# Kernel optimization log

Measured on AMD Instinct MI355X. Metric: run time of the kernel, lower is better.

The kernel has to match this reference:

```python
import jax, jax.numpy as jnp
import numpy as np

H = 128  # GRU hidden size


def gru_cell(x_t, h, W_ih, W_hh, b_ih, b_hh):
    # Standard torch GRU cell math.
    gi = x_t @ W_ih.T + b_ih            # (bs, 3H)
    gh = h @ W_hh.T + b_hh              # (bs, 3H)
    i_r, i_z, i_n = jnp.split(gi, 3, axis=-1)
    h_r, h_z, h_n = jnp.split(gh, 3, axis=-1)
    r = jax.nn.sigmoid(i_r + h_r)
    z = jax.nn.sigmoid(i_z + h_z)
    n = jnp.tanh(i_n + r * h_n)
    return (1.0 - z) * n + z * h


def setup_inputs() -> dict:
    key = jax.random.key(0)
    ks = jax.random.split(key, 16)
    bs, seq, emb, nc = 64, 1024, 300, 23
    s = 0.05
    inp = {
        "x": jax.random.normal(ks[0], (bs, seq, emb), jnp.float32),
        "adj": jax.random.uniform(ks[1], (bs, seq, seq), jnp.float32),
        "mask": jax.random.uniform(ks[2], (bs, seq, 1), jnp.float32),
        # GRU forward direction params (torch layout: W_ih (3H, emb), W_hh (3H, H))
        "W_ih_f": jax.random.normal(ks[3], (3 * H, emb), jnp.float32) * s,
        "W_hh_f": jax.random.normal(ks[4], (3 * H, H), jnp.float32) * s,
        "b_ih_f": jax.random.normal(ks[5], (3 * H,), jnp.float32) * s,
        "b_hh_f": jax.random.normal(ks[6], (3 * H,), jnp.float32) * s,
        # GRU backward direction params
        "W_ih_b": jax.random.normal(ks[7], (3 * H, emb), jnp.float32) * s,
        "W_hh_b": jax.random.normal(ks[8], (3 * H, H), jnp.float32) * s,
        "b_ih_b": jax.random.normal(ks[9], (3 * H,), jnp.float32) * s,
        "b_hh_b": jax.random.normal(ks[10], (3 * H,), jnp.float32) * s,
        # MLP head: Linear(300+256,128) -> Linear(128,64) -> Linear(64,23)
        "W1": jax.random.normal(ks[11], (128, emb + 2 * H), jnp.float32) * s,
        "b1": jnp.zeros((128,), jnp.float32),
        "W2": jax.random.normal(ks[12], (64, 128), jnp.float32) * s,
        "b2": jnp.zeros((64,), jnp.float32),
        "W3": jax.random.normal(ks[13], (nc, 64), jnp.float32) * s,
        "b3": jnp.zeros((nc,), jnp.float32),
    }
    return inp


def reference(x, adj, mask, W_ih_f, W_hh_f, b_ih_f, b_hh_f,
              W_ih_b, W_hh_b, b_ih_b, b_hh_b, W1, b1, W2, b2, W3, b3):
    x = x * mask                                   # (bs, seq, emb)
    bs, seq, emb = x.shape

    # --- bidirectional GRU, last-step output ---
    # Forward direction output at t = seq-1 is the final hidden of a full scan.
    h0 = jnp.zeros((bs, H), x.dtype)
    def step(h, x_t):
        h_new = gru_cell(x_t, h, W_ih_f, W_hh_f, b_ih_f, b_hh_f)
        return h_new, None
    h_fwd, _ = jax.lax.scan(step, h0, jnp.swapaxes(x, 0, 1))  # (bs, H)
    # Backward direction output at t = seq-1 is exactly ONE cell step on x[:, -1]
    # starting from the zero initial state (it has only consumed the last token).
    h_bwd = gru_cell(x[:, -1, :], h0, W_ih_b, W_hh_b, b_ih_b, b_hh_b)
    h = jnp.concatenate([h_fwd, h_bwd], axis=1)    # (bs, 2H)

    # --- gfm: sum_{i,j} x_i * x_j per feature == (sum_i x_i)^2 ---
    # (original code materializes a (bs, seq*seq, emb) tensor; adj is dead code)
    s = jnp.sum(x, axis=1)                         # (bs, emb)
    gfm = s * s                                    # (bs, emb)

    # --- MLP head (dropout is identity at eval) ---
    z = jnp.concatenate([h, gfm], axis=1)          # (bs, 2H + emb)
    z = jax.nn.relu(z @ W1.T + b1)
    z = jax.nn.relu(z @ W2.T + b2)
    logit = z @ W3.T + b3                          # (bs, num_class)
    return logit
```

## Files before the change

kernel.cpp:

```cpp
#include <hip/hip_runtime.h>
#include <hip/hip_bf16.h>

#define HH   128
#define EMB  300
#define SEQ  1024
#define BS   64
#define NG   384
#define NCHUNK 8

typedef __attribute__((ext_vector_type(8))) short  bf16x8;
typedef __attribute__((ext_vector_type(4))) float  f32x4;
typedef _Float16 f16x2 __attribute__((ext_vector_type(2)));

__device__ __forceinline__ unsigned short f2bf(float f) {
    unsigned int u = __float_as_uint(f);
    unsigned int r = (u + 0x7fffu + ((u >> 16) & 1u)) >> 16;
    return (unsigned short)r;
}
__device__ __forceinline__ float fexp(float x) { return __builtin_amdgcn_exp2f(x * 1.44269504088896f); }
__device__ __forceinline__ float fsig(float x) { return __builtin_amdgcn_rcpf(1.f + fexp(-x)); }
__device__ __forceinline__ float ftanh(float x){ return __builtin_amdgcn_rcpf(1.f + fexp(-2.f*x)) * 2.f - 1.f; }

__device__ __forceinline__ float dpp_pair_add(float x) {
    int y = __builtin_amdgcn_mov_dpp(__float_as_int(x), 0xB1, 0xF, 0xF, true);
    return x + __int_as_float(y);
}

#define BAR_LDS() asm volatile("s_waitcnt lgkmcnt(0)\n\ts_barrier" ::: "memory")

__global__ __launch_bounds__(512) void gi_gemm(const float* __restrict__ X,
                                               const float* __restrict__ mask,
                                               const float* __restrict__ W,
                                               const float* __restrict__ bias,
                                               const float* __restrict__ bhh2,
                                               float* __restrict__ out) {
    __shared__ __align__(16) unsigned short As[128 * 32];
    __shared__ __align__(16) unsigned short Bs[384 * 32];
    const int m0   = blockIdx.x * 128;
    const int tid  = threadIdx.x;
    const int row  = tid >> 2;
    const int seg  = tid & 3;
    const int wave = tid >> 6;
    const int lane = tid & 63;
    const int wm   = wave >> 2;
    const int wn   = wave & 3;
    const int r16  = lane & 15, kg = lane >> 4;

    f32x4 acc[4][6];
    #pragma unroll
    for (int m = 0; m < 4; ++m)
        #pragma unroll
        for (int n = 0; n < 6; ++n) acc[m][n] = (f32x4){0.f,0.f,0.f,0.f};

    const float mrow = mask[m0 + row];

    for (int k0 = 0; k0 < 320; k0 += 32) {
        {
            const float* src = X + (size_t)(m0 + row) * EMB + k0 + seg * 8;
            unsigned short tmp[8];
            if (k0 + seg * 8 + 7 < EMB) {
                float4 v0 = ((const float4*)src)[0];
                float4 v1 = ((const float4*)src)[1];
                tmp[0]=f2bf(v0.x*mrow); tmp[1]=f2bf(v0.y*mrow);
                tmp[2]=f2bf(v0.z*mrow); tmp[3]=f2bf(v0.w*mrow);
                tmp[4]=f2bf(v1.x*mrow); tmp[5]=f2bf(v1.y*mrow);
                tmp[6]=f2bf(v1.z*mrow); tmp[7]=f2bf(v1.w*mrow);
            } else {
                #pragma unroll
                for (int i = 0; i < 8; ++i) {
                    int c = k0 + seg * 8 + i;
                    float v = (c < EMB) ? src[i] : 0.f;
                    tmp[i] = f2bf(v * mrow);
                }
            }
            *(uint4*)&As[row * 32 + seg * 8] = *(const uint4*)tmp;
        }
        #pragma unroll
        for (int r3 = 0; r3 < 3; ++r3) {
            const int rowb = row + r3 * 128;
            const float* src = W + (size_t)rowb * EMB + k0 + seg * 8;
            unsigned short tmp[8];
            if (k0 + seg * 8 + 7 < EMB) {
                float4 v0 = ((const float4*)src)[0];
                float4 v1 = ((const float4*)src)[1];
                tmp[0]=f2bf(v0.x); tmp[1]=f2bf(v0.y); tmp[2]=f2bf(v0.z); tmp[3]=f2bf(v0.w);
                tmp[4]=f2bf(v1.x); tmp[5]=f2bf(v1.y); tmp[6]=f2bf(v1.z); tmp[7]=f2bf(v1.w);
            } else {
                #pragma unroll
                for (int i = 0; i < 8; ++i) {
                    int c = k0 + seg * 8 + i;
                    float v = (c < EMB) ? src[i] : 0.f;
                    tmp[i] = f2bf(v);
                }
            }
            *(uint4*)&Bs[rowb * 32 + seg * 8] = *(const uint4*)tmp;
        }
        __syncthreads();

        bf16x8 a[4], bfr[6];
        #pragma unroll
        for (int m = 0; m < 4; ++m)
            a[m] = *(const bf16x8*)&As[(wm * 64 + m * 16 + r16) * 32 + kg * 8];
        #pragma unroll
        for (int n = 0; n < 6; ++n)
            bfr[n] = *(const bf16x8*)&Bs[(wn * 96 + n * 16 + r16) * 32 + kg * 8];
        #pragma unroll
        for (int m = 0; m < 4; ++m)
            #pragma unroll
            for (int n = 0; n < 6; ++n)
                acc[m][n] = __builtin_amdgcn_mfma_f32_16x16x32_bf16(a[m], bfr[n], acc[m][n], 0, 0, 0);
        __syncthreads();
    }

    #pragma unroll
    for (int m = 0; m < 4; ++m) {
        const int rowb = m0 + wm * 64 + m * 16 + kg * 4;
        #pragma unroll
        for (int n = 0; n < 6; ++n) {
            const int col = wn * 96 + n * 16 + r16;
            const float bj = bias[col] + (col < 2 * HH ? bhh2[col] : 0.f);
            #pragma unroll
            for (int q = 0; q < 4; ++q)
                out[(size_t)(rowb + q) * NG + col] = acc[m][n][q] + bj;
        }
    }
}

__global__ __launch_bounds__(320) void col_sum(const float* __restrict__ X,
                                               const float* __restrict__ mask,
                                               float* __restrict__ spart) {
    const int b = blockIdx.x, c = blockIdx.y;
    const int e = threadIdx.x;
    if (e >= EMB) return;
    const int tchunk = SEQ / NCHUNK;
    float acc = 0.f;
    const float* xb = X + ((size_t)b * SEQ + (size_t)c * tchunk) * EMB;
    const float* mb = mask + (size_t)b * SEQ + (size_t)c * tchunk;
    for (int t = 0; t < tchunk; ++t)
        acc += xb[(size_t)t * EMB + e] * mb[t];
    spart[((size_t)b * NCHUNK + c) * EMB + e] = acc;
}

__global__ __launch_bounds__(256, 1) void gru_scan(const float* __restrict__ gi,
                                                   const float* __restrict__ Whh,
                                                   const float* __restrict__ bhh,
                                                   float* __restrict__ hout) {
    const int b    = blockIdx.x;
    const int tid  = threadIdx.x;
    const int j    = tid >> 1;
    const int half = tid & 1;
    __shared__ __align__(16) _Float16 hb[2][HH];

    f16x2 wr_[32], wz_[32], wn_[32];
    {
        const float2* r0 = (const float2*)(Whh + (size_t)j * HH            + half * 64);
        const float2* r1 = (const float2*)(Whh + (size_t)(j + HH) * HH     + half * 64);
        const float2* r2 = (const float2*)(Whh + (size_t)(j + 2 * HH) * HH + half * 64);
        #pragma unroll
        for (int i = 0; i < 32; ++i) {
            float2 a = r0[i], c = r1[i], d = r2[i];
            wr_[i] = (f16x2){(_Float16)a.x, (_Float16)a.y};
            wz_[i] = (f16x2){(_Float16)c.x, (_Float16)c.y};
            wn_[i] = (f16x2){(_Float16)d.x, (_Float16)d.y};
        }
    }
    const float bn_ = bhh[j + 2 * HH];

    float hreg = 0.f;
    if (tid < HH) hb[0][tid] = (_Float16)0.f;
    const float* gb = gi + (size_t)b * SEQ * NG;

    float gAr, gAz, gAn, gBr, gBz, gBn, gCr, gCz, gCn, gDr, gDz, gDn;
    {
        const float* g0 = gb;               gAr = g0[j]; gAz = g0[j+HH]; gAn = g0[j+2*HH];
        const float* g1 = gb + NG;          gBr = g1[j]; gBz = g1[j+HH]; gBn = g1[j+2*HH];
        const float* g2 = gb + 2 * NG;      gCr = g2[j]; gCz = g2[j+HH]; gCn = g2[j+2*HH];
        const float* g3 = gb + 3 * NG;      gDr = g3[j]; gDz = g3[j+HH]; gDn = g3[j+2*HH];
    }
    const float* pA = gb + 4 * NG;
    const float* pB = gb + 5 * NG;
    const float* pC = gb + 6 * NG;
    const float* pD = gb + 7 * NG;
    BAR_LDS();

    const f16x2 Z2 = (f16x2){(_Float16)0.f, (_Float16)0.f};

#define GRU_BODY(P, GR, GZ, GN, PP)                                            \
    {                                                                          \
        f16x2 ar0=Z2, ar1=Z2, ar2=Z2, ar3=Z2;                                  \
        f16x2 az0=Z2, az1=Z2, az2=Z2, az3=Z2;                                  \
        f16x2 an0=Z2, an1=Z2, an2=Z2, an3=Z2;                                  \
        const uint4* hp = (const uint4*)&hb[P][half * 64];                     \
        _Pragma("unroll")                                                      \
        for (int i = 0; i < 8; ++i) {                                          \
            union { uint4 u; f16x2 h2[4]; } U;                                 \
            U.u = hp[i];                                                       \
            ar0 = wr_[i*4+0] * U.h2[0] + ar0;                                  \
            ar1 = wr_[i*4+1] * U.h2[1] + ar1;                                  \
            ar2 = wr_[i*4+2] * U.h2[2] + ar2;                                  \
            ar3 = wr_[i*4+3] * U.h2[3] + ar3;                                  \
            az0 = wz_[i*4+0] * U.h2[0] + az0;                                  \
            az1 = wz_[i*4+1] * U.h2[1] + az1;                                  \
            az2 = wz_[i*4+2] * U.h2[2] + az2;                                  \
            az3 = wz_[i*4+3] * U.h2[3] + az3;                                  \
            an0 = wn_[i*4+0] * U.h2[0] + an0;                                  \
            an1 = wn_[i*4+1] * U.h2[1] + an1;                                  \
            an2 = wn_[i*4+2] * U.h2[2] + an2;                                  \
            an3 = wn_[i*4+3] * U.h2[3] + an3;                                  \
        }                                                                      \
        f16x2 sr = (ar0 + ar1) + (ar2 + ar3);                                  \
        f16x2 sz = (az0 + az1) + (az2 + az3);                                  \
        f16x2 sn = (an0 + an1) + (an2 + an3);                                  \
        const float arf = dpp_pair_add((float)sr[0] + (float)sr[1]);           \
        const float azf = dpp_pair_add((float)sz[0] + (float)sz[1]);           \
        const float anf = dpp_pair_add((float)sn[0] + (float)sn[1]);           \
        const float r = fsig(GR + arf);                                        \
        const float z = fsig(GZ + azf);                                        \
        const float n = ftanh(GN + r * (anf + bn_));                           \
        hreg = n + z * (hreg - n);                                             \
        if (!half) hb[P ^ 1][j] = (_Float16)hreg;                              \
        GR = PP[j]; GZ = PP[j + HH]; GN = PP[j + 2 * HH];                      \
        PP += 4 * NG;                                                          \
        BAR_LDS();                                                             \
    }

    for (int it = 0; it < SEQ / 4; ++it) {
        GRU_BODY(0, gAr, gAz, gAn, pA)
        GRU_BODY(1, gBr, gBz, gBn, pB)
        GRU_BODY(0, gCr, gCz, gCn, pC)
        GRU_BODY(1, gDr, gDz, gDn, pD)
    }
#undef GRU_BODY
    if (!half) hout[b * HH + j] = hreg;
}

__global__ __launch_bounds__(128) void mlp(const float* __restrict__ X,
                                           const float* __restrict__ mask,
                                           const float* __restrict__ WihB,
                                           const float* __restrict__ bihB,
                                           const float* __restrict__ bhhB,
                                           const float* __restrict__ hf,
                                           const float* __restrict__ spart,
                                           const float* __restrict__ W1, const float* __restrict__ b1,
                                           const float* __restrict__ W2, const float* __restrict__ b2,
                                           const float* __restrict__ W3, const float* __restrict__ b3,
                                           float* __restrict__ out) {
    const int b = blockIdx.x, j = threadIdx.x;
    __shared__ float xl[EMB];
    __shared__ float zin[2 * HH + EMB];
    __shared__ float l1[128];
    __shared__ float l2[64];

    const float* xr = X + ((size_t)b * SEQ + (SEQ - 1)) * EMB;
    const float  mv = mask[(size_t)b * SEQ + SEQ - 1];
    for (int e = j; e < EMB; e += 128) xl[e] = xr[e];
    zin[j] = hf[b * HH + j];
    for (int e = j; e < EMB; e += 128) {
        float v = 0.f;
        #pragma unroll
        for (int c = 0; c < NCHUNK; ++c)
            v += spart[((size_t)b * NCHUNK + c) * EMB + e];
        zin[2 * HH + e] = v * v;
    }
    __syncthreads();

    {
        const float* wR = WihB + (size_t)j * EMB;
        const float* wZ = WihB + (size_t)(j + HH) * EMB;
        const float* wN = WihB + (size_t)(j + 2 * HH) * EMB;
        float aR = 0.f, aZ = 0.f, aN = 0.f;
        for (int e = 0; e < EMB; ++e) {
            const float xv = xl[e];
            aR += xv * wR[e]; aZ += xv * wZ[e]; aN += xv * wN[e];
        }
        const float r = fsig(aR * mv + bihB[j] + bhhB[j]);
        const float z = fsig(aZ * mv + bihB[j + HH] + bhhB[j + HH]);
        const float n = ftanh(aN * mv + bihB[j + 2 * HH] + r * bhhB[j + 2 * HH]);
        zin[HH + j] = (1.f - z) * n;
    }
    __syncthreads();

    {
        float a = b1[j];
        const float* w = W1 + (size_t)j * (2 * HH + EMB);
        for (int i = 0; i < 2 * HH + EMB; ++i) a += zin[i] * w[i];
        l1[j] = fmaxf(a, 0.f);
    }
    __syncthreads();
    if (j < 64) {
        float a = b2[j];
        const float* w = W2 + (size_t)j * 128;
        for (int i = 0; i < 128; ++i) a += l1[i] * w[i];
        l2[j] = fmaxf(a, 0.f);
    }
    __syncthreads();
    if (j < 23) {
        float a = b3[j];
        const float* w = W3 + (size_t)j * 64;
        for (int i = 0; i < 64; ++i) a += l2[i] * w[i];
        out[b * 23 + j] = a;
    }
}

extern "C" void kernel_launch(void* const* d_in, const int* in_sizes, int n_in,
                              void* d_out, int out_size, void* d_ws, size_t ws_size,
                              hipStream_t stream) {
    const float* x     = (const float*)d_in[0];
    const float* mask  = (const float*)d_in[2];
    const float* Wih_f = (const float*)d_in[3];
    const float* Whh_f = (const float*)d_in[4];
    const float* bih_f = (const float*)d_in[5];
    const float* bhh_f = (const float*)d_in[6];
    const float* Wih_b = (const float*)d_in[7];
    const float* bih_b = (const float*)d_in[9];
    const float* bhh_b = (const float*)d_in[10];
    const float* W1 = (const float*)d_in[11];
    const float* b1 = (const float*)d_in[12];
    const float* W2 = (const float*)d_in[13];
    const float* b2 = (const float*)d_in[14];
    const float* W3 = (const float*)d_in[15];
    const float* b3 = (const float*)d_in[16];
    float* out = (float*)d_out;

    float* gi    = (float*)d_ws;
    float* spart = gi + (size_t)BS * SEQ * NG;
    float* hf    = spart + (size_t)BS * NCHUNK * EMB;

    gi_gemm<<<dim3(512), dim3(512), 0, stream>>>(x, mask, Wih_f, bih_f, bhh_f, gi);
    col_sum<<<dim3(BS, NCHUNK), dim3(320), 0, stream>>>(x, mask, spart);
    gru_scan<<<dim3(BS), dim3(256), 0, stream>>>(gi, Whh_f, bhh_f, hf);
    mlp<<<dim3(BS), dim3(128), 0, stream>>>(x, mask, Wih_b, bih_b, bhh_b, hf, spart,
                                            W1, b1, W2, b2, W3, b3, out);
}
```

Before: 577.6 us.

## Split GRU recurrent dot products four ways and use fdot2 with fp32 accumulation

Rewrites the per-step recurrent matvec in the GRU scan. Each group of four threads now computes two hidden units (j and j+64) over quarter-length slices of h, and the reduction uses a two-stage DPP quad sum. The packed f16 FMAs are replaced with v_dot2 f16 instructions that accumulate in fp32. The goal is a shorter dependent chain per step and better accuracy, at the cost of duplicated gate math and a select across the two units.

```diff
diff --git a/kernel.cpp b/kernel.cpp
--- a/kernel.cpp
+++ b/kernel.cpp
@@ -21,9 +21,11 @@
 __device__ __forceinline__ float fsig(float x) { return __builtin_amdgcn_rcpf(1.f + fexp(-x)); }
 __device__ __forceinline__ float ftanh(float x){ return __builtin_amdgcn_rcpf(1.f + fexp(-2.f*x)) * 2.f - 1.f; }
 
-__device__ __forceinline__ float dpp_pair_add(float x) {
-    int y = __builtin_amdgcn_mov_dpp(__float_as_int(x), 0xB1, 0xF, 0xF, true);
-    return x + __int_as_float(y);
+__device__ __forceinline__ float dpp_quad_sum(float x) {
+    int a = __builtin_amdgcn_mov_dpp(__float_as_int(x), 0xB1, 0xF, 0xF, true);
+    float s = x + __int_as_float(a);
+    int c = __builtin_amdgcn_mov_dpp(__float_as_int(s), 0x4E, 0xF, 0xF, true);
+    return s + __int_as_float(c);
 }
 
 #define BAR_LDS() asm volatile("s_waitcnt lgkmcnt(0)\n\ts_barrier" ::: "memory")
@@ -145,26 +147,34 @@
                                                    const float* __restrict__ Whh,
                                                    const float* __restrict__ bhh,
                                                    float* __restrict__ hout) {
-    const int b    = blockIdx.x;
-    const int tid  = threadIdx.x;
-    const int j    = tid >> 1;
-    const int half = tid & 1;
+    const int b   = blockIdx.x;
+    const int tid = threadIdx.x;
+    const int jj  = tid >> 2;
+    const int q   = tid & 3;
+    const int jg  = jj + ((q >> 1) << 6);
     __shared__ __align__(16) _Float16 hb[2][HH];
 
-    f16x2 wr_[32], wz_[32], wn_[32];
+    f16x2 wAr[16], wAz[16], wAn[16], wBr[16], wBz[16], wBn[16];
     {
-        const float2* r0 = (const float2*)(Whh + (size_t)j * HH            + half * 64);
-        const float2* r1 = (const float2*)(Whh + (size_t)(j + HH) * HH     + half * 64);
-        const float2* r2 = (const float2*)(Whh + (size_t)(j + 2 * HH) * HH + half * 64);
-        #pragma unroll
-        for (int i = 0; i < 32; ++i) {
-            float2 a = r0[i], c = r1[i], d = r2[i];
-            wr_[i] = (f16x2){(_Float16)a.x, (_Float16)a.y};
-            wz_[i] = (f16x2){(_Float16)c.x, (_Float16)c.y};
-            wn_[i] = (f16x2){(_Float16)d.x, (_Float16)d.y};
-        }
-    }
-    const float bn_ = bhh[j + 2 * HH];
+        const float2* a0 = (const float2*)(Whh + (size_t)jj * HH                 + q * 32);
+        const float2* a1 = (const float2*)(Whh + (size_t)(jj + HH) * HH          + q * 32);
+        const float2* a2 = (const float2*)(Whh + (size_t)(jj + 2 * HH) * HH      + q * 32);
+        const float2* b0 = (const float2*)(Whh + (size_t)(jj + 64) * HH          + q * 32);
+        const float2* b1 = (const float2*)(Whh + (size_t)(jj + 64 + HH) * HH     + q * 32);
+        const float2* b2 = (const float2*)(Whh + (size_t)(jj + 64 + 2 * HH) * HH + q * 32);
+        #pragma unroll
+        for (int i = 0; i < 16; ++i) {
+            float2 v;
+            v = a0[i]; wAr[i] = (f16x2){(_Float16)v.x, (_Float16)v.y};
+            v = a1[i]; wAz[i] = (f16x2){(_Float16)v.x, (_Float16)v.y};
+            v = a2[i]; wAn[i] = (f16x2){(_Float16)v.x, (_Float16)v.y};
+            v = b0[i]; wBr[i] = (f16x2){(_Float16)v.x, (_Float16)v.y};
+            v = b1[i]; wBz[i] = (f16x2){(_Float16)v.x, (_Float16)v.y};
+            v = b2[i]; wBn[i] = (f16x2){(_Float16)v.x, (_Float16)v.y};
+        }
+    }
+    const float bn_ = bhh[jg + 2 * HH];
+    const bool  ownA = (q < 2);
 
     float hreg = 0.f;
     if (tid < HH) hb[0][tid] = (_Float16)0.f;
@@ -172,10 +182,10 @@
 
     float gAr, gAz, gAn, gBr, gBz, gBn, gCr, gCz, gCn, gDr, gDz, gDn;
     {
-        const float* g0 = gb;               gAr = g0[j]; gAz = g0[j+HH]; gAn = g0[j+2*HH];
-        const float* g1 = gb + NG;          gBr = g1[j]; gBz = g1[j+HH]; gBn = g1[j+2*HH];
-        const float* g2 = gb + 2 * NG;      gCr = g2[j]; gCz = g2[j+HH]; gCn = g2[j+2*HH];
-        const float* g3 = gb + 3 * NG;      gDr = g3[j]; gDz = g3[j+HH]; gDn = g3[j+2*HH];
+        const float* g0 = gb;               gAr = g0[jg]; gAz = g0[jg+HH]; gAn = g0[jg+2*HH];
+        const float* g1 = gb + NG;          gBr = g1[jg]; gBz = g1[jg+HH]; gBn = g1[jg+2*HH];
+        const float* g2 = gb + 2 * NG;      gCr = g2[jg]; gCz = g2[jg+HH]; gCn = g2[jg+2*HH];
+        const float* g3 = gb + 3 * NG;      gDr = g3[jg]; gDz = g3[jg+HH]; gDn = g3[jg+2*HH];
     }
     const float* pA = gb + 4 * NG;
     const float* pB = gb + 5 * NG;
@@ -183,43 +193,41 @@
     const float* pD = gb + 7 * NG;
     BAR_LDS();
 
-    const f16x2 Z2 = (f16x2){(_Float16)0.f, (_Float16)0.f};
-
 #define GRU_BODY(P, GR, GZ, GN, PP)                                            \
     {                                                                          \
-        f16x2 ar0=Z2, ar1=Z2, ar2=Z2, ar3=Z2;                                  \
-        f16x2 az0=Z2, az1=Z2, az2=Z2, az3=Z2;                                  \
-        f16x2 an0=Z2, an1=Z2, an2=Z2, an3=Z2;                                  \
-        const uint4* hp = (const uint4*)&hb[P][half * 64];                     \
+        float arA[2]={0.f,0.f}, azA[2]={0.f,0.f}, anA[2]={0.f,0.f};            \
+        float arB[2]={0.f,0.f}, azB[2]={0.f,0.f}, anB[2]={0.f,0.f};            \
+        const uint4* hp = (const uint4*)&hb[P][q * 32];                        \
         _Pragma("unroll")                                                      \
-        for (int i = 0; i < 8; ++i) {                                          \
+        for (int i = 0; i < 4; ++i) {                                          \
             union { uint4 u; f16x2 h2[4]; } U;                                 \
             U.u = hp[i];                                                       \
-            ar0 = wr_[i*4+0] * U.h2[0] + ar0;                                  \
-            ar1 = wr_[i*4+1] * U.h2[1] + ar1;                                  \
-            ar2 = wr_[i*4+2] * U.h2[2] + ar2;                                  \
-            ar3 = wr_[i*4+3] * U.h2[3] + ar3;                                  \
-            az0 = wz_[i*4+0] * U.h2[0] + az0;                                  \
-            az1 = wz_[i*4+1] * U.h2[1] + az1;                                  \
-            az2 = wz_[i*4+2] * U.h2[2] + az2;                                  \
-            az3 = wz_[i*4+3] * U.h2[3] + az3;                                  \
-            an0 = wn_[i*4+0] * U.h2[0] + an0;                                  \
-            an1 = wn_[i*4+1] * U.h2[1] + an1;                                  \
-            an2 = wn_[i*4+2] * U.h2[2] + an2;                                  \
-            an3 = wn_[i*4+3] * U.h2[3] + an3;                                  \
+            _Pragma("unroll")                                                  \
+            for (int k = 0; k < 4; ++k) {                                      \
+                const int c = k & 1;                                           \
+                arA[c] = __builtin_amdgcn_fdot2(wAr[i*4+k], U.h2[k], arA[c], false); \
+                azA[c] = __builtin_amdgcn_fdot2(wAz[i*4+k], U.h2[k], azA[c], false); \
+                anA[c] = __builtin_amdgcn_fdot2(wAn[i*4+k], U.h2[k], anA[c], false); \
+                arB[c] = __builtin_amdgcn_fdot2(wBr[i*4+k], U.h2[k], arB[c], false); \
+                azB[c] = __builtin_amdgcn_fdot2(wBz[i*4+k], U.h2[k], azB[c], false); \
+                anB[c] = __builtin_amdgcn_fdot2(wBn[i*4+k], U.h2[k], anB[c], false); \
+            }                                                                  \
         }                                                                      \
-        f16x2 sr = (ar0 + ar1) + (ar2 + ar3);                                  \
-        f16x2 sz = (az0 + az1) + (az2 + az3);                                  \
-        f16x2 sn = (an0 + an1) + (an2 + an3);                                  \
-        const float arf = dpp_pair_add((float)sr[0] + (float)sr[1]);           \
-        const float azf = dpp_pair_add((float)sz[0] + (float)sz[1]);           \
-        const float anf = dpp_pair_add((float)sn[0] + (float)sn[1]);           \
+        const float sArf = dpp_quad_sum(arA[0] + arA[1]);                      \
+        const float sAzf = dpp_quad_sum(azA[0] + azA[1]);                      \
+        const float sAnf = dpp_quad_sum(anA[0] + anA[1]);                      \
+        const float sBrf = dpp_quad_sum(arB[0] + arB[1]);                      \
+        const float sBzf = dpp_quad_sum(azB[0] + azB[1]);                      \
+        const float sBnf = dpp_quad_sum(anB[0] + anB[1]);                      \
+        const float arf = ownA ? sArf : sBrf;                                  \
+        const float azf = ownA ? sAzf : sBzf;                                  \
+        const float anf = ownA ? sAnf : sBnf;                                  \
         const float r = fsig(GR + arf);                                        \
         const float z = fsig(GZ + azf);                                        \
         const float n = ftanh(GN + r * (anf + bn_));                           \
         hreg = n + z * (hreg - n);                                             \
-        if (!half) hb[P ^ 1][j] = (_Float16)hreg;                              \
-        GR = PP[j]; GZ = PP[j + HH]; GN = PP[j + 2 * HH];                      \
+        if (!(q & 1)) hb[P ^ 1][jg] = (_Float16)hreg;                          \
+        GR = PP[jg]; GZ = PP[jg + HH]; GN = PP[jg + 2 * HH];                   \
         PP += 4 * NG;                                                          \
         BAR_LDS();                                                             \
     }
@@ -231,7 +239,7 @@
         GRU_BODY(1, gDr, gDz, gDn, pD)
     }
 #undef GRU_BODY
-    if (!half) hout[b * HH + j] = hreg;
+    if (!(q & 1)) hout[b * HH + jg] = hreg;
 }
 
 __global__ __launch_bounds__(128) void mlp(const float* __restrict__ X,
```

Measured after the change: 540.9 us. 1.07x faster.
